# Kernel tuning notes

Measured on AMD Instinct MI355X. Metric: run time of the kernel, lower is better.

The kernel has to match this reference:

```python
import jax, jax.numpy as jnp
import numpy as np

K = 3  # Chebyshev order (number of coefficients)


def setup_inputs() -> dict:
    key = jax.random.key(0)
    k1, k2, k3, k4 = jax.random.split(key, 4)
    B, nNode, c_in, T = 16, 512, 32, 64
    c_out = 64
    x = jax.random.normal(k1, (B, nNode, c_in, T), dtype=jnp.float32)
    # scaled Laplacian-like batched adjacency; scale keeps the Chebyshev
    # recursion numerically tame (spectral norm ~ O(1))
    adj = jax.random.normal(k2, (B, nNode, nNode), dtype=jnp.float32) * (1.0 / np.sqrt(nNode))
    # 1x1 conv params: weight [c_out, K*c_in], bias [c_out]
    W = jax.random.normal(k3, (c_out, K * c_in), dtype=jnp.float32) * 0.1
    b = jax.random.normal(k4, (c_out,), dtype=jnp.float32) * 0.1
    return {"x": x, "adj": adj, "W": W, "b": b}


def reference(x, adj, W, b):
    # x: [B, nNode, c_in, T] -> permute(0,2,1,3) -> [B, c_in, nNode, T]
    x = jnp.transpose(x, (0, 2, 1, 3))
    B, c_in, nNode, T = x.shape
    # Chebyshev recursion: L0 = I, L1 = adj, L_k = 2*adj@L_{k-1} - L_{k-2}
    L0 = jnp.broadcast_to(jnp.eye(nNode, dtype=x.dtype), (B, nNode, nNode))
    L1 = adj
    Ls = [L0, L1]
    for _ in range(2, K):
        L2 = 2.0 * jnp.matmul(adj, L1) - L0
        L0, L1 = L1, L2
        Ls.append(L2)
    Lap = jnp.stack(Ls, axis=1)              # [B, K, nNode, nNode]
    Lap = jnp.swapaxes(Lap, -1, -2)          # transpose(-1, -2)
    # einsum 'bcnl,bknq->bckql' then view [B, c_in*K, nNode, T]
    y = jnp.einsum('bcnl,bknq->bckql', x, Lap)  # [B, c_in, K, nNode, T]
    y = y.reshape(B, c_in * K, nNode, T)
    # 1x1 Conv2d: channel mixing + bias
    out = jnp.einsum('oc,bcnl->bonl', W, y) + b[None, :, None, None]
    return out
```

## Files before the change

### kernel.cpp

```cpp
#include <hip/hip_runtime.h>

typedef unsigned short u16;
typedef __bf16 v8bf __attribute__((ext_vector_type(8)));
typedef float f32x4 __attribute__((ext_vector_type(4)));
typedef u16 us8 __attribute__((ext_vector_type(8)));
typedef u16 us4 __attribute__((ext_vector_type(4)));

static __device__ __forceinline__ u16 f2bf(float f) {
  union { __bf16 h; u16 u; } cv;
  cv.h = (__bf16)f;
  return cv.u;
}

static __device__ __forceinline__ void gl_lds16(const u16* g, u16* l) {
  __builtin_amdgcn_global_load_lds(
      (const __attribute__((address_space(1))) unsigned int*)g,
      (__attribute__((address_space(3))) unsigned int*)l, 16, 0, 0);
}

__global__ __launch_bounds__(256)
void cvt_adj_foldw_k(const float* __restrict__ adj, u16* __restrict__ adj_bf,
                     const float* __restrict__ W, u16* __restrict__ Mb) {
  if (blockIdx.x < 2048) {
    const int i = blockIdx.x * 256 + threadIdx.x;
    const float4 a = ((const float4*)adj)[2 * i];
    const float4 b = ((const float4*)adj)[2 * i + 1];
    us8 r;
    r[0] = f2bf(a.x); r[1] = f2bf(a.y); r[2] = f2bf(a.z); r[3] = f2bf(a.w);
    r[4] = f2bf(b.x); r[5] = f2bf(b.y); r[6] = f2bf(b.z); r[7] = f2bf(b.w);
    ((us8*)adj_bf)[i] = r;
  } else {
    for (int i = threadIdx.x; i < 64 * 96; i += 256) {
      const int cc = i % 96;
      const int r = cc % 3;
      const float w = W[i];
      const float m = (r == 0) ? (w - W[i + 2]) : ((r == 1) ? w : 2.0f * w);
      Mb[i] = f2bf(m);
    }
  }
}

__global__ __launch_bounds__(256)
void cvtT_x_k(const float* __restrict__ x, u16* __restrict__ xT) {
  const int j0 = blockIdx.x * 64;
  const int q0 = blockIdx.y * 64;
  const int b = blockIdx.z;
  __shared__ u16 Ls[64][68];
  const int tid = threadIdx.x;
#pragma unroll
  for (int i = 0; i < 4; ++i) {
    const int idx = tid + 256 * i;
    const int r = idx >> 4;
    const int j4 = (idx & 15) * 4;
    const float4 v = *(const float4*)(x + ((size_t)(b * 512 + q0 + r) * 2048 + j0 + j4));
    us4 o;
    o[0] = f2bf(v.x); o[1] = f2bf(v.y); o[2] = f2bf(v.z); o[3] = f2bf(v.w);
    *(us4*)&Ls[r][j4] = o;
  }
  __syncthreads();
#pragma unroll
  for (int i = 0; i < 2; ++i) {
    const int idx = tid + 256 * i;
    const int rp = idx >> 3;
    const int q8 = (idx & 7) * 8;
    us8 o;
#pragma unroll
    for (int j = 0; j < 8; ++j) o[j] = Ls[q8 + j][rp];
    *(us8*)(xT + ((size_t)(b * 2048 + j0 + rp) * 512 + q0 + q8)) = o;
  }
}

template<bool WT>
__global__ __launch_bounds__(256)
void gemm_t(const u16* __restrict__ A, const u16* __restrict__ BT,
            u16* __restrict__ C, u16* __restrict__ CT) {
  const int b = blockIdx.z;
  const int row0 = blockIdx.y * 128;
  const int col0 = blockIdx.x * 128;
  const u16* Ab = A + (size_t)b * 512 * 512;
  const u16* BTb = BT + (size_t)b * 2048 * 512;

  __shared__ u16 smem[17408];
  u16* As = smem;
  u16* Bs = smem + 8192;

  const int tid = threadIdx.x;
  const int lane = tid & 63;
  const int w = tid >> 6;
  const int wm = (w >> 1) * 64;
  const int wn = (w & 1) * 64;
  const int l16 = lane & 15;
  const int kg = lane >> 4;

  f32x4 acc[4][4];
#pragma unroll
  for (int m = 0; m < 4; ++m)
#pragma unroll
    for (int n = 0; n < 4; ++n) acc[m][n] = (f32x4){0.f, 0.f, 0.f, 0.f};

  for (int k0 = 0; k0 < 512; k0 += 64) {
    __syncthreads();
#pragma unroll
    for (int i = 0; i < 4; ++i) {
      const int eb = w * 2048 + i * 512;
      const int e = eb + lane * 8;
      const int r = e >> 6;
      const int kk = e & 63;
      gl_lds16(Ab + (size_t)(row0 + r) * 512 + k0 + kk, As + eb);
      gl_lds16(BTb + (size_t)(col0 + r) * 512 + k0 + kk, Bs + eb);
    }
    __syncthreads();
#pragma unroll
    for (int ks = 0; ks < 2; ++ks) {
      v8bf af[4], bfr[4];
#pragma unroll
      for (int m = 0; m < 4; ++m)
        af[m] = *(const v8bf*)(As + (wm + m * 16 + l16) * 64 + ks * 32 + kg * 8);
#pragma unroll
      for (int n = 0; n < 4; ++n)
        bfr[n] = *(const v8bf*)(Bs + (wn + n * 16 + l16) * 64 + ks * 32 + kg * 8);
#pragma unroll
      for (int m = 0; m < 4; ++m)
#pragma unroll
        for (int n = 0; n < 4; ++n)
          acc[m][n] = __builtin_amdgcn_mfma_f32_16x16x32_bf16(af[m], bfr[n], acc[m][n], 0, 0, 0);
    }
  }

  u16* Cb = C + (size_t)b * 512 * 2048;
#pragma unroll
  for (int m = 0; m < 4; ++m)
#pragma unroll
    for (int n = 0; n < 4; ++n)
#pragma unroll
      for (int v = 0; v < 4; ++v) {
        const int rr = row0 + wm + m * 16 + kg * 4 + v;
        const int cc = col0 + wn + n * 16 + l16;
        Cb[(size_t)rr * 2048 + cc] = f2bf(acc[m][n][v]);
      }

  if constexpr (WT) {
    __syncthreads();
    u16* Ctr = smem;
#pragma unroll
    for (int m = 0; m < 4; ++m)
#pragma unroll
      for (int n = 0; n < 4; ++n)
#pragma unroll
        for (int v = 0; v < 4; ++v)
          Ctr[(wn + n * 16 + l16) * 136 + (wm + m * 16 + kg * 4 + v)] = f2bf(acc[m][n][v]);
    __syncthreads();
    u16* CTb = CT + (size_t)b * 2048 * 512;
#pragma unroll
    for (int i = 0; i < 8; ++i) {
      const int idx = tid + 256 * i;
      const int jp = idx >> 4;
      const int q8 = (idx & 15) * 8;
      const us8 o = *(const us8*)(Ctr + jp * 136 + q8);
      *(us8*)(CTb + (size_t)(col0 + jp) * 512 + row0 + q8) = o;
    }
  }
}

__global__ __launch_bounds__(256)
void mix_mfma(const float* __restrict__ x0, const u16* __restrict__ x1,
              const u16* __restrict__ y2, const u16* __restrict__ Mb,
              const float* __restrict__ bias, float* __restrict__ out) {
  const int q = blockIdx.x;
  const int b = blockIdx.y;
  __shared__ u16 Vt[64][104];
  __shared__ u16 Ms[64][104];
  const int tid = threadIdx.x;
  const int lane = tid & 63;
  const int w = tid >> 6;
  const int l16 = lane & 15;
  const int kg = lane >> 4;

#pragma unroll
  for (int i = 0; i < 3; ++i) {
    const int idx = tid + 256 * i;
    const int o = idx / 12;
    const int c8 = (idx % 12) * 8;
    *(uint4*)&Ms[o][c8] = *(const uint4*)(Mb + o * 96 + c8);
  }
  const size_t base = ((size_t)b * 512 + q) * 2048;
#pragma unroll
  for (int i = 0; i < 2; ++i) {
    const int idx = tid + 256 * i;
    const int c = idx >> 4;
    const int l0 = (idx & 15) * 4;
    const float4 v = *(const float4*)(x0 + base + c * 64 + l0);
    Vt[l0 + 0][3 * c] = f2bf(v.x);
    Vt[l0 + 1][3 * c] = f2bf(v.y);
    Vt[l0 + 2][3 * c] = f2bf(v.z);
    Vt[l0 + 3][3 * c] = f2bf(v.w);
  }
  {
    const int c = tid >> 3;
    const int l0 = (tid & 7) * 8;
    const us8 v1 = *(const us8*)(x1 + base + c * 64 + l0);
    const us8 v2 = *(const us8*)(y2 + base + c * 64 + l0);
#pragma unroll
    for (int j = 0; j < 8; ++j) {
      Vt[l0 + j][3 * c + 1] = v1[j];
      Vt[l0 + j][3 * c + 2] = v2[j];
    }
  }
  __syncthreads();

  f32x4 acc[4];
#pragma unroll
  for (int n = 0; n < 4; ++n) acc[n] = (f32x4){0.f, 0.f, 0.f, 0.f};
#pragma unroll
  for (int ks = 0; ks < 3; ++ks) {
    const v8bf a = *(const v8bf*)&Ms[w * 16 + l16][ks * 32 + kg * 8];
#pragma unroll
    for (int n = 0; n < 4; ++n) {
      const v8bf bv = *(const v8bf*)&Vt[n * 16 + l16][ks * 32 + kg * 8];
      acc[n] = __builtin_amdgcn_mfma_f32_16x16x32_bf16(a, bv, acc[n], 0, 0, 0);
    }
  }
#pragma unroll
  for (int n = 0; n < 4; ++n)
#pragma unroll
    for (int v = 0; v < 4; ++v) {
      const int o = w * 16 + kg * 4 + v;
      out[(((size_t)b * 64 + o) * 512 + q) * 64 + n * 16 + l16] = acc[n][v] + bias[o];
    }
}

extern "C" void kernel_launch(void* const* d_in, const int* in_sizes, int n_in,
                              void* d_out, int out_size, void* d_ws, size_t ws_size,
                              hipStream_t stream) {
  const float* x   = (const float*)d_in[0];
  const float* adj = (const float*)d_in[1];
  const float* W   = (const float*)d_in[2];
  const float* bia = (const float*)d_in[3];
  float* out = (float*)d_out;

  u16* adj_bf = (u16*)d_ws;
  u16* xT     = adj_bf + (size_t)16 * 512 * 512;
  u16* X1     = xT     + (size_t)16 * 2048 * 512;
  u16* X1T    = X1     + (size_t)16 * 512 * 2048;
  u16* Y2     = X1T    + (size_t)16 * 2048 * 512;
  u16* Mb     = Y2     + (size_t)16 * 512 * 2048;

  hipLaunchKernelGGL(cvt_adj_foldw_k, dim3(2049), dim3(256), 0, stream, adj, adj_bf, W, Mb);
  hipLaunchKernelGGL(cvtT_x_k, dim3(32, 8, 16), dim3(256), 0, stream, x, xT);

  dim3 gg(2048 / 128, 512 / 128, 16);
  hipLaunchKernelGGL((gemm_t<true>), gg, dim3(256), 0, stream, adj_bf, xT, X1, X1T);
  hipLaunchKernelGGL((gemm_t<false>), gg, dim3(256), 0, stream, adj_bf, X1T, Y2, (u16*)nullptr);

  hipLaunchKernelGGL(mix_mfma, dim3(512, 16), dim3(256), 0, stream, x, X1, Y2, Mb, bia, out);
}
```

Before: 158.5 us.

## Precompute 2·adj² and fuse both Chebyshev propagations into one dual-GEMM kernel

```diff
diff --git a/kernel.cpp b/kernel.cpp
--- a/kernel.cpp
+++ b/kernel.cpp
@@ -19,22 +19,42 @@
 }
 
 __global__ __launch_bounds__(256)
-void cvt_adj_foldw_k(const float* __restrict__ adj, u16* __restrict__ adj_bf,
-                     const float* __restrict__ W, u16* __restrict__ Mb) {
-  if (blockIdx.x < 2048) {
-    const int i = blockIdx.x * 256 + threadIdx.x;
-    const float4 a = ((const float4*)adj)[2 * i];
-    const float4 b = ((const float4*)adj)[2 * i + 1];
-    us8 r;
-    r[0] = f2bf(a.x); r[1] = f2bf(a.y); r[2] = f2bf(a.z); r[3] = f2bf(a.w);
-    r[4] = f2bf(b.x); r[5] = f2bf(b.y); r[6] = f2bf(b.z); r[7] = f2bf(b.w);
-    ((us8*)adj_bf)[i] = r;
-  } else {
-    for (int i = threadIdx.x; i < 64 * 96; i += 256) {
+void cvt_adjT_foldw_k(const float* __restrict__ adj, u16* __restrict__ adj_bf,
+                      u16* __restrict__ adjT_bf, const float* __restrict__ W,
+                      u16* __restrict__ Mb) {
+  const int c0 = blockIdx.x * 64;
+  const int r0 = blockIdx.y * 64;
+  const int b = blockIdx.z;
+  __shared__ u16 Ls[64][68];
+  const int tid = threadIdx.x;
+#pragma unroll
+  for (int i = 0; i < 4; ++i) {
+    const int idx = tid + 256 * i;
+    const int r = idx >> 4;
+    const int c4 = (idx & 15) * 4;
+    const float4 v = *(const float4*)(adj + ((size_t)(b * 512 + r0 + r) * 512 + c0 + c4));
+    us4 o;
+    o[0] = f2bf(v.x); o[1] = f2bf(v.y); o[2] = f2bf(v.z); o[3] = f2bf(v.w);
+    *(us4*)&Ls[r][c4] = o;
+    *(us4*)(adj_bf + ((size_t)(b * 512 + r0 + r) * 512 + c0 + c4)) = o;
+  }
+  __syncthreads();
+#pragma unroll
+  for (int i = 0; i < 2; ++i) {
+    const int idx = tid + 256 * i;
+    const int c = idx >> 3;
+    const int r8 = (idx & 7) * 8;
+    us8 o;
+#pragma unroll
+    for (int j = 0; j < 8; ++j) o[j] = Ls[r8 + j][c];
+    *(us8*)(adjT_bf + ((size_t)(b * 512 + c0 + c) * 512 + r0 + r8)) = o;
+  }
+  if (blockIdx.x == 0 && blockIdx.y == 0 && blockIdx.z == 0) {
+    for (int i = tid; i < 64 * 96; i += 256) {
       const int cc = i % 96;
       const int r = cc % 3;
       const float w = W[i];
-      const float m = (r == 0) ? (w - W[i + 2]) : ((r == 1) ? w : 2.0f * w);
+      const float m = (r == 0) ? (w - W[i + 2]) : w;
       Mb[i] = f2bf(m);
     }
   }
@@ -61,26 +81,25 @@
 #pragma unroll
   for (int i = 0; i < 2; ++i) {
     const int idx = tid + 256 * i;
-    const int rp = idx >> 3;
+    const int jp = idx >> 3;
     const int q8 = (idx & 7) * 8;
     us8 o;
 #pragma unroll
-    for (int j = 0; j < 8; ++j) o[j] = Ls[q8 + j][rp];
-    *(us8*)(xT + ((size_t)(b * 2048 + j0 + rp) * 512 + q0 + q8)) = o;
-  }
-}
-
-template<bool WT>
-__global__ __launch_bounds__(256)
-void gemm_t(const u16* __restrict__ A, const u16* __restrict__ BT,
-            u16* __restrict__ C, u16* __restrict__ CT) {
+    for (int j = 0; j < 8; ++j) o[j] = Ls[q8 + j][jp];
+    *(us8*)(xT + ((size_t)(b * 2048 + j0 + jp) * 512 + q0 + q8)) = o;
+  }
+}
+
+__global__ __launch_bounds__(256)
+void gemm_sq(const u16* __restrict__ A, const u16* __restrict__ BT,
+             u16* __restrict__ C) {
   const int b = blockIdx.z;
   const int row0 = blockIdx.y * 128;
   const int col0 = blockIdx.x * 128;
   const u16* Ab = A + (size_t)b * 512 * 512;
-  const u16* BTb = BT + (size_t)b * 2048 * 512;
-
-  __shared__ u16 smem[17408];
+  const u16* BTb = BT + (size_t)b * 512 * 512;
+
+  __shared__ u16 smem[16384];
   u16* As = smem;
   u16* Bs = smem + 8192;
 
@@ -126,8 +145,7 @@
           acc[m][n] = __builtin_amdgcn_mfma_f32_16x16x32_bf16(af[m], bfr[n], acc[m][n], 0, 0, 0);
     }
   }
-
-  u16* Cb = C + (size_t)b * 512 * 2048;
+  u16* Cb = C + (size_t)b * 512 * 512;
 #pragma unroll
   for (int m = 0; m < 4; ++m)
 #pragma unroll
@@ -136,30 +154,94 @@
       for (int v = 0; v < 4; ++v) {
         const int rr = row0 + wm + m * 16 + kg * 4 + v;
         const int cc = col0 + wn + n * 16 + l16;
-        Cb[(size_t)rr * 2048 + cc] = f2bf(acc[m][n][v]);
+        Cb[(size_t)rr * 512 + cc] = f2bf(2.0f * acc[m][n][v]);
       }
-
-  if constexpr (WT) {
+}
+
+__global__ __launch_bounds__(256)
+void prop_k(const u16* __restrict__ A1, const u16* __restrict__ A2,
+            const u16* __restrict__ BT, u16* __restrict__ X1,
+            u16* __restrict__ Y2) {
+  const int b = blockIdx.z;
+  const int row0 = blockIdx.y * 128;
+  const int col0 = blockIdx.x * 128;
+  const u16* A1b = A1 + (size_t)b * 512 * 512;
+  const u16* A2b = A2 + (size_t)b * 512 * 512;
+  const u16* BTb = BT + (size_t)b * 2048 * 512;
+
+  __shared__ u16 smem[24576];
+  u16* As1 = smem;
+  u16* As2 = smem + 8192;
+  u16* Bs  = smem + 16384;
+
+  const int tid = threadIdx.x;
+  const int lane = tid & 63;
+  const int w = tid >> 6;
+  const int wm = (w >> 1) * 64;
+  const int wn = (w & 1) * 64;
+  const int l16 = lane & 15;
+  const int kg = lane >> 4;
+
+  f32x4 accA[4][4], accB[4][4];
+#pragma unroll
+  for (int m = 0; m < 4; ++m)
+#pragma unroll
+    for (int n = 0; n < 4; ++n) {
+      accA[m][n] = (f32x4){0.f, 0.f, 0.f, 0.f};
+      accB[m][n] = (f32x4){0.f, 0.f, 0.f, 0.f};
+    }
+
+  for (int k0 = 0; k0 < 512; k0 += 64) {
     __syncthreads();
-    u16* Ctr = smem;
-#pragma unroll
-    for (int m = 0; m < 4; ++m)
+#pragma unroll
+    for (int i = 0; i < 4; ++i) {
+      const int eb = w * 2048 + i * 512;
+      const int e = eb + lane * 8;
+      const int r = e >> 6;
+      const int kk = e & 63;
+      gl_lds16(A1b + (size_t)(row0 + r) * 512 + k0 + kk, As1 + eb);
+      gl_lds16(A2b + (size_t)(row0 + r) * 512 + k0 + kk, As2 + eb);
+      gl_lds16(BTb + (size_t)(col0 + r) * 512 + k0 + kk, Bs + eb);
+    }
+    __syncthreads();
+#pragma unroll
+    for (int ks = 0; ks < 2; ++ks) {
+      v8bf bfr[4], af[4];
 #pragma unroll
       for (int n = 0; n < 4; ++n)
-#pragma unroll
-        for (int v = 0; v < 4; ++v)
-          Ctr[(wn + n * 16 + l16) * 136 + (wm + m * 16 + kg * 4 + v)] = f2bf(acc[m][n][v]);
-    __syncthreads();
-    u16* CTb = CT + (size_t)b * 2048 * 512;
-#pragma unroll
-    for (int i = 0; i < 8; ++i) {
-      const int idx = tid + 256 * i;
-      const int jp = idx >> 4;
-      const int q8 = (idx & 15) * 8;
-      const us8 o = *(const us8*)(Ctr + jp * 136 + q8);
-      *(us8*)(CTb + (size_t)(col0 + jp) * 512 + row0 + q8) = o;
-    }
-  }
+        bfr[n] = *(const v8bf*)(Bs + (wn + n * 16 + l16) * 64 + ks * 32 + kg * 8);
+#pragma unroll
+      for (int m = 0; m < 4; ++m)
+        af[m] = *(const v8bf*)(As1 + (wm + m * 16 + l16) * 64 + ks * 32 + kg * 8);
+#pragma unroll
+      for (int m = 0; m < 4; ++m)
+#pragma unroll
+        for (int n = 0; n < 4; ++n)
+          accA[m][n] = __builtin_amdgcn_mfma_f32_16x16x32_bf16(af[m], bfr[n], accA[m][n], 0, 0, 0);
+#pragma unroll
+      for (int m = 0; m < 4; ++m)
+        af[m] = *(const v8bf*)(As2 + (wm + m * 16 + l16) * 64 + ks * 32 + kg * 8);
+#pragma unroll
+      for (int m = 0; m < 4; ++m)
+#pragma unroll
+        for (int n = 0; n < 4; ++n)
+          accB[m][n] = __builtin_amdgcn_mfma_f32_16x16x32_bf16(af[m], bfr[n], accB[m][n], 0, 0, 0);
+    }
+  }
+
+  u16* X1b = X1 + (size_t)b * 512 * 2048;
+  u16* Y2b = Y2 + (size_t)b * 512 * 2048;
+#pragma unroll
+  for (int m = 0; m < 4; ++m)
+#pragma unroll
+    for (int n = 0; n < 4; ++n)
+#pragma unroll
+      for (int v = 0; v < 4; ++v) {
+        const int rr = row0 + wm + m * 16 + kg * 4 + v;
+        const int cc = col0 + wn + n * 16 + l16;
+        X1b[(size_t)rr * 2048 + cc] = f2bf(accA[m][n][v]);
+        Y2b[(size_t)rr * 2048 + cc] = f2bf(accB[m][n][v]);
+      }
 }
 
 __global__ __launch_bounds__(256)
@@ -238,19 +320,21 @@
   const float* bia = (const float*)d_in[3];
   float* out = (float*)d_out;
 
-  u16* adj_bf = (u16*)d_ws;
-  u16* xT     = adj_bf + (size_t)16 * 512 * 512;
-  u16* X1     = xT     + (size_t)16 * 2048 * 512;
-  u16* X1T    = X1     + (size_t)16 * 512 * 2048;
-  u16* Y2     = X1T    + (size_t)16 * 2048 * 512;
-  u16* Mb     = Y2     + (size_t)16 * 512 * 2048;
-
-  hipLaunchKernelGGL(cvt_adj_foldw_k, dim3(2049), dim3(256), 0, stream, adj, adj_bf, W, Mb);
+  u16* adj_bf  = (u16*)d_ws;
+  u16* adjT_bf = adj_bf  + (size_t)16 * 512 * 512;
+  u16* adj2_bf = adjT_bf + (size_t)16 * 512 * 512;
+  u16* xT      = adj2_bf + (size_t)16 * 512 * 512;
+  u16* X1      = xT      + (size_t)16 * 2048 * 512;
+  u16* Y2      = X1      + (size_t)16 * 512 * 2048;
+  u16* Mb      = Y2      + (size_t)16 * 512 * 2048;
+
+  hipLaunchKernelGGL(cvt_adjT_foldw_k, dim3(8, 8, 16), dim3(256), 0, stream,
+                     adj, adj_bf, adjT_bf, W, Mb);
   hipLaunchKernelGGL(cvtT_x_k, dim3(32, 8, 16), dim3(256), 0, stream, x, xT);
-
-  dim3 gg(2048 / 128, 512 / 128, 16);
-  hipLaunchKernelGGL((gemm_t<true>), gg, dim3(256), 0, stream, adj_bf, xT, X1, X1T);
-  hipLaunchKernelGGL((gemm_t<false>), gg, dim3(256), 0, stream, adj_bf, X1T, Y2, (u16*)nullptr);
-
-  hipLaunchKernelGGL(mix_mfma, dim3(512, 16), dim3(256), 0, stream, x, X1, Y2, Mb, bia, out);
-}
+  hipLaunchKernelGGL(gemm_sq, dim3(4, 4, 16), dim3(256), 0, stream,
+                     adj_bf, adjT_bf, adj2_bf);
+  hipLaunchKernelGGL(prop_k, dim3(16, 4, 16), dim3(256), 0, stream,
+                     adj_bf, adj2_bf, xT, X1, Y2);
+  hipLaunchKernelGGL(mix_mfma, dim3(512, 16), dim3(256), 0, stream,
+                     x, X1, Y2, Mb, bia, out);
+}
```

Measured after the change: 173.9 us. 1.1x slower.
